# Optimization experiments

Measured on AMD Instinct MI355X. Metric: run time of the kernel, lower is better.

The kernel has to match this reference:

```python
import jax, jax.numpy as jnp
import numpy as np

B = 8192        # number of drug-cell pairs (graphs)
NPG = 32        # nodes per graph
EPG = 64        # directed edges per graph
N = B * NPG     # total nodes
E = B * EPG     # total edges
CELL = 908      # cell_inp_dim
BN_EPS = 1e-5


def _bn(x):
    # BatchNorm1d in training mode with gamma=1, beta=0 (fresh init), biased var
    m = x.mean(0)
    v = x.var(0)
    return (x - m) * jax.lax.rsqrt(v + BN_EPS)


def _lin_params(k, fan_in, fan_out):
    kw, _ = jax.random.split(k)
    w = jax.random.normal(kw, (fan_in, fan_out), jnp.float32) / np.sqrt(fan_in)
    b = jnp.zeros((fan_out,), jnp.float32)
    return w, b


_DIMS = [("ce_1", CELL, 516), ("ce_2", 516, 256), ("ce_3", 256, 128),
         ("g1_1", 9, 128), ("g1_2", 128, 128),
         ("g2_1", 128, 128), ("g2_2", 128, 128),
         ("d_1", 128, 128), ("d_2", 128, 128),
         ("f_1", 256, 128), ("f_2", 128, 64), ("f_3", 64, 1)]


def setup_inputs() -> dict:
    key = jax.random.key(0)
    ks = jax.random.split(key, 4 + len(_DIMS))
    inp = {}
    inp["cell"] = jax.random.normal(ks[0], (B, CELL), jnp.float32)
    inp["drug_x"] = jax.random.normal(ks[1], (N, 9), jnp.float32)
    g = jnp.arange(E) // EPG  # graph id per edge
    src = g * NPG + jax.random.randint(ks[2], (E,), 0, NPG)
    dst = g * NPG + jax.random.randint(ks[3], (E,), 0, NPG)
    inp["drug_edge_index"] = jnp.stack([src, dst]).astype(jnp.int32)
    inp["drug_batch"] = (jnp.arange(N) // NPG).astype(jnp.int32)
    for i, (nm, a, b) in enumerate(_DIMS):
        w, bb = _lin_params(ks[4 + i], a, b)
        inp[nm + "_w"] = w
        inp[nm + "_b"] = bb
    return inp


def _forward(cell, drug_x, src, dst, batch,
             ce_1_w, ce_1_b, ce_2_w, ce_2_b, ce_3_w, ce_3_b,
             g1_1_w, g1_1_b, g1_2_w, g1_2_b,
             g2_1_w, g2_1_b, g2_2_w, g2_2_b,
             d_1_w, d_1_b, d_2_w, d_2_b,
             f_1_w, f_1_b, f_2_w, f_2_b, f_3_w, f_3_b):
    # cell_emb branch (dropout = identity in eval/reference)
    c = jax.nn.relu(_bn(cell @ ce_1_w + ce_1_b))
    c = jax.nn.relu(_bn(c @ ce_2_w + ce_2_b))
    c = jax.nn.relu(_bn(c @ ce_3_w + ce_3_b))

    # GINConv 1: h = MLP((1+eps)*x + sum_{j in N(i)} x_j), eps=0
    agg = jax.ops.segment_sum(drug_x[src], dst, num_segments=N)
    h = drug_x + agg
    h = jax.nn.relu(_bn(h @ g1_1_w + g1_1_b)) @ g1_2_w + g1_2_b  # inner MLP: Lin-BN-ReLU-Lin
    h = _bn(jax.nn.relu(h))  # outer ReLU then BN (per Sequential order)

    # GINConv 2
    agg = jax.ops.segment_sum(h[src], dst, num_segments=N)
    h = h + agg
    h = jax.nn.relu(_bn(h @ g2_1_w + g2_1_b)) @ g2_2_w + g2_2_b
    h = _bn(jax.nn.relu(h))

    # global max pool over nodes of each graph -> [B, 128]
    p = jax.ops.segment_max(h, batch, num_segments=B)

    d = jax.nn.relu(_bn(p @ d_1_w + d_1_b))
    d = jax.nn.relu(d @ d_2_w + d_2_b)

    z = jnp.concatenate([c, d], axis=-1)  # [B, 256]
    z = jax.nn.elu(_bn(z @ f_1_w + f_1_b))
    z = jax.nn.elu(_bn(z @ f_2_w + f_2_b))
    y = (z @ f_3_w + f_3_b).reshape(B)
    return y


def reference(cell, drug_x, drug_edge_index, drug_batch,
              ce_1_w, ce_1_b, ce_2_w, ce_2_b, ce_3_w, ce_3_b,
              g1_1_w, g1_1_b, g1_2_w, g1_2_b,
              g2_1_w, g2_1_b, g2_2_w, g2_2_b,
              d_1_w, d_1_b, d_2_w, d_2_b,
              f_1_w, f_1_b, f_2_w, f_2_b, f_3_w, f_3_b):
    src, dst = drug_edge_index[0], drug_edge_index[1]
    return _forward(cell, drug_x, src, dst, drug_batch,
                    ce_1_w, ce_1_b, ce_2_w, ce_2_b, ce_3_w, ce_3_b,
                    g1_1_w, g1_1_b, g1_2_w, g1_2_b,
                    g2_1_w, g2_1_b, g2_2_w, g2_2_b,
                    d_1_w, d_1_b, d_2_w, d_2_b,
                    f_1_w, f_1_b, f_2_w, f_2_b, f_3_w, f_3_b)
```

## Files before the change

### kernel.cpp

```cpp
#include <hip/hip_runtime.h>
#include <hip/hip_bf16.h>
#include <math.h>

#define BGRAPH 8192
#define NPG 32
#define EPG 64
#define NNODE (BGRAPH * NPG)
#define NEDGE (BGRAPH * EPG)
#define CELLD 908
#define BN_EPS 1e-5f
#define ABF_STR 1024
#define C1_STR 640

typedef __attribute__((ext_vector_type(8))) short bf16x8;
typedef __attribute__((ext_vector_type(4))) float f32x4;
typedef __attribute__((ext_vector_type(4))) unsigned short us4;
typedef __attribute__((ext_vector_type(8))) unsigned short us8;

__device__ __forceinline__ unsigned short f2bf(float f)
{
    unsigned int u = __float_as_uint(f);
    u = (u + 0x7FFFu + ((u >> 16) & 1u)) >> 16;
    return (unsigned short)u;
}

__device__ __forceinline__ bf16x8 quant8(const float v[8])
{
    union { bf16x8 b; unsigned short u[8]; } fr;
    #pragma unroll
    for (int j = 0; j < 8; ++j) fr.u[j] = f2bf(v[j]);
    return fr.b;
}

__device__ __forceinline__ void bf2f8(bf16x8 b, float v[8])
{
    union { bf16x8 bb; unsigned short u[8]; } x; x.bb = b;
    #pragma unroll
    for (int j = 0; j < 8; ++j) v[j] = __uint_as_float((unsigned)x.u[j] << 16);
}

__device__ __forceinline__ float apply_in(float v, int mode, float mn, float iv)
{
    if (mode == 1)      { v = (v - mn) * iv; v = fmaxf(v, 0.f); }
    else if (mode == 2) { v = (v - mn) * iv; v = (v > 0.f) ? v : expm1f(v); }
    else if (mode == 3) { v = fmaxf(v, 0.f); v = (v - mn) * iv; }
    return v;
}

struct TransArgs {
    const float* w[11];
    unsigned short* wt[11];
    int K[11], N[11], ntN[11];
    int off[12];
};

__global__ void transpose_w(TransArgs a)
{
    __shared__ float t[64][65];
    int b = blockIdx.x, tid = threadIdx.x;
    int s = 0;
    while (s < 10 && b >= a.off[s + 1]) ++s;
    int t0 = b - a.off[s];
    int K = a.K[s], N = a.N[s], ntn = a.ntN[s];
    int kt = t0 / ntn, nt = t0 - kt * ntn;
    int k0 = kt * 64, n0 = nt * 64;
    const float* w = a.w[s];
    unsigned short* wt = a.wt[s];
    int c = tid & 63, rg = tid >> 6;
    #pragma unroll
    for (int i = 0; i < 16; ++i) {
        int rr = rg * 16 + i;
        int k = k0 + rr, n = n0 + c;
        t[c][rr] = (k < K && n < N) ? w[(size_t)k * N + n] : 0.f;
    }
    __syncthreads();
    #pragma unroll
    for (int i = 0; i < 16; ++i) {
        int rr = rg * 16 + i;
        int n = n0 + rr, k = k0 + c;
        if (n < N && k < K) wt[(size_t)n * K + k] = f2bf(t[rr][c]);
    }
}

struct SetupArgs {
    float* zb; int zTotal; int zBlocks;
    const int* src; const int* dst; int* row_start; int* col_idx;
};

__global__ void setup_all(SetupArgs a)
{
    int b = blockIdx.x;
    int tid = threadIdx.x;
    if (b < a.zBlocks) {
        int i = b * 256 + tid;
        if (i < a.zTotal) a.zb[i] = 0.f;
        return;
    }
    b -= a.zBlocks;
    __shared__ int cnt[4][32], fill[4][32], rsl[4][33];
    int gl = tid >> 6, e = tid & 63;
    int g = b * 4 + gl;
    if (e < 32) { cnt[gl][e] = 0; fill[gl][e] = 0; }
    __syncthreads();
    int s = a.src[g * EPG + e] - g * NPG;
    int d = a.dst[g * EPG + e] - g * NPG;
    atomicAdd(&cnt[gl][d], 1);
    __syncthreads();
    if (e == 0) {
        int acc = 0;
        for (int i = 0; i < 32; ++i) { rsl[gl][i] = acc; acc += cnt[gl][i]; }
        rsl[gl][32] = acc;
    }
    __syncthreads();
    int pos = rsl[gl][d] + atomicAdd(&fill[gl][d], 1);
    a.col_idx[g * EPG + pos] = s;
    if (e < 33) a.row_start[g * 33 + e] = rsl[gl][e];
}

__global__ void quant_cell(const float* __restrict__ cell, unsigned short* __restrict__ abf)
{
    int i = blockIdx.x * 256 + threadIdx.x;
    int row = i / (ABF_STR / 4), c4 = i - row * (ABF_STR / 4);
    int k = c4 * 4;
    us4 w = (us4){0, 0, 0, 0};
    if (k < CELLD) {
        float4 f = *(const float4*)&cell[(size_t)row * CELLD + k];
        w = (us4){ f2bf(f.x), f2bf(f.y), f2bf(f.z), f2bf(f.w) };
    }
    *(us4*)&abf[(size_t)row * ABF_STR + k] = w;
}

__global__ void quant_c1(const float* __restrict__ c1, const float* __restrict__ stats,
                         float inv_sM, unsigned short* __restrict__ out)
{
    int i = blockIdx.x * 256 + threadIdx.x;
    int row = i / (C1_STR / 4), c4 = i - row * (C1_STR / 4);
    int k = c4 * 4;
    us4 w = (us4){0, 0, 0, 0};
    if (k < 516) {
        float4 f = *(const float4*)&c1[(size_t)row * 516 + k];
        float v[4] = {f.x, f.y, f.z, f.w};
        #pragma unroll
        for (int j = 0; j < 4; ++j) {
            float s = stats[k + j], ss = stats[516 + k + j];
            float mn = s * inv_sM;
            float iv = rsqrtf(ss * inv_sM - mn * mn + BN_EPS);
            v[j] = fmaxf((v[j] - mn) * iv, 0.f);
        }
        w = (us4){ f2bf(v[0]), f2bf(v[1]), f2bf(v[2]), f2bf(v[3]) };
    }
    *(us4*)&out[(size_t)row * C1_STR + k] = w;
}

__global__ void reduce_stats(const float* __restrict__ part, int nrows, int nt,
                             float* __restrict__ out)
{
    int c = threadIdx.x;
    int per = nrows >> 6;
    int r0 = blockIdx.x * per;
    bool isq = (c >= 128);
    int cc = isq ? c - 128 : c;
    if (cc >= nt) return;
    float s = 0.f;
    for (int r = 0; r < per; ++r) s += part[(size_t)(r0 + r) * 256 + c];
    unsafeAtomicAdd(&out[(isq ? nt : 0) + cc], s);
}

#define HBS 136

__launch_bounds__(256)
__global__ void gin_s1(const float* __restrict__ drug_x,
                       const int* __restrict__ row_start,
                       const int* __restrict__ col_idx,
                       const unsigned short* __restrict__ W11,
                       const float* __restrict__ b11,
                       unsigned short* uout,
                       float* __restrict__ part)
{
    __shared__ __align__(16) unsigned short h[4 * 32 * HBS];
    __shared__ __align__(16) unsigned char ubuf[4096];
    __shared__ int rs[4][36];
    __shared__ int ci[4][64];

    unsigned short* w11l = (unsigned short*)ubuf;
    float* red = (float*)ubuf;

    int tid  = threadIdx.x;
    int wave = tid >> 6;
    int lane = tid & 63;
    int quad = lane >> 4;
    int l16  = lane & 15;
    int g0   = blockIdx.x * 4;
    unsigned short* hw = h + wave * (32 * HBS);
    float* xw = (float*)hw;

    for (int i = tid; i < 128 * 16; i += 256) {
        int n = i >> 4, k = i & 15;
        w11l[i] = (k < 9) ? W11[n * 9 + k] : (unsigned short)0;
    }
    if (tid < 132) {
        int gl = tid / 33, idx = tid - gl * 33;
        rs[gl][idx] = row_start[(g0 + gl) * 33 + idx];
    }
    {
        int gl = tid >> 6, e = tid & 63;
        ci[gl][e] = col_idx[(g0 + gl) * EPG + e];
    }
    {
        const float* xg = drug_x + (size_t)(g0 + wave) * 32 * 9;
        for (int i = lane; i < 32 * 16; i += 64) {
            int rr = i >> 4, c = i & 15;
            xw[i] = (c < 9) ? xg[rr * 9 + c] : 0.f;
        }
    }
    __syncthreads();

    f32x4 acc[2][8];
    #pragma unroll
    for (int i = 0; i < 2; ++i)
        #pragma unroll
        for (int j = 0; j < 8; ++j)
            acc[i][j] = (f32x4){0.f, 0.f, 0.f, 0.f};

    {
        bf16x8 af[2];
        #pragma unroll
        for (int mt = 0; mt < 2; ++mt) {
            int rowl = mt * 16 + l16;
            float v[8] = {0, 0, 0, 0, 0, 0, 0, 0};
            if (quad < 2) {
                float4 lo = *(const float4*)&xw[rowl * 16 + quad * 8];
                float4 hi = *(const float4*)&xw[rowl * 16 + quad * 8 + 4];
                v[0] = lo.x; v[1] = lo.y; v[2] = lo.z; v[3] = lo.w;
                v[4] = hi.x; v[5] = hi.y; v[6] = hi.z; v[7] = hi.w;
                int e0 = rs[wave][rowl], e1 = rs[wave][rowl + 1];
                for (int e = e0; e < e1; ++e) {
                    int sr = ci[wave][e];
                    float4 l2 = *(const float4*)&xw[sr * 16 + quad * 8];
                    float4 h2 = *(const float4*)&xw[sr * 16 + quad * 8 + 4];
                    v[0] += l2.x; v[1] += l2.y; v[2] += l2.z; v[3] += l2.w;
                    v[4] += h2.x; v[5] += h2.y; v[6] += h2.z; v[7] += h2.w;
                }
            }
            af[mt] = quant8(v);
        }
        #pragma unroll
        for (int nt = 0; nt < 8; ++nt) {
            bf16x8 b;
            if (quad < 2) b = *(const bf16x8*)(const void*)&w11l[(nt * 16 + l16) * 16 + quad * 8];
            else { float z[8] = {0,0,0,0,0,0,0,0}; b = quant8(z); }
            acc[0][nt] = __builtin_amdgcn_mfma_f32_16x16x32_bf16(af[0], b, acc[0][nt], 0, 0, 0);
            acc[1][nt] = __builtin_amdgcn_mfma_f32_16x16x32_bf16(af[1], b, acc[1][nt], 0, 0, 0);
        }
    }

    float ls[8], lq[8];
    unsigned short* ub = uout + (size_t)(g0 + wave) * 32 * 128;
    #pragma unroll
    for (int nt = 0; nt < 8; ++nt) {
        int col = nt * 16 + l16;
        float bv = b11[col];
        float s0 = 0.f, q0 = 0.f;
        #pragma unroll
        for (int mt = 0; mt < 2; ++mt) {
            int rb = mt * 16 + quad * 4;
            #pragma unroll
            for (int r = 0; r < 4; ++r) {
                float u = acc[mt][nt][r] + bv;
                ub[(size_t)(rb + r) * 128 + col] = f2bf(u);
                s0 += u; q0 += u * u;
            }
        }
        ls[nt] = s0; lq[nt] = q0;
    }
    __syncthreads();
    #pragma unroll
    for (int nt = 0; nt < 8; ++nt) {
        float s = ls[nt], q = lq[nt];
        s += __shfl_xor(s, 16); q += __shfl_xor(q, 16);
        s += __shfl_xor(s, 32); q += __shfl_xor(q, 32);
        if (quad == 0) {
            int col = nt * 16 + l16;
            red[(wave * 2 + 0) * 128 + col] = s;
            red[(wave * 2 + 1) * 128 + col] = q;
        }
    }
    __syncthreads();
    if (tid < 128) {
        float s = red[0 * 128 + tid] + red[2 * 128 + tid] + red[4 * 128 + tid] + red[6 * 128 + tid];
        float q = red[1 * 128 + tid] + red[3 * 128 + tid] + red[5 * 128 + tid] + red[7 * 128 + tid];
        part[(size_t)blockIdx.x * 256 + tid] = s;
        part[(size_t)blockIdx.x * 256 + 128 + tid] = q;
    }
}

__launch_bounds__(256)
__global__ void gin_s3f(const unsigned short* __restrict__ uin,
                        const int* __restrict__ row_start,
                        const int* __restrict__ col_idx,
                        const unsigned short* __restrict__ Wt,
                        const float* __restrict__ bias,
                        const float* __restrict__ in_stats, float inv_sM,
                        unsigned short* __restrict__ uout,
                        float* __restrict__ part)
{
    __shared__ __align__(16) unsigned short wsl[128 * 136];
    __shared__ float pmv[256];
    __shared__ int rs[2][33];
    __shared__ int ci[2][64];
    float* zt = (float*)wsl;

    int tid  = threadIdx.x;
    int wave = tid >> 6;
    int lane = tid & 63;
    int quad = lane >> 4;
    int l16  = lane & 15;
    int g0   = blockIdx.x * 2;
    int row0 = blockIdx.x * 64;

    if (tid < 128) {
        float s = in_stats[tid], ss = in_stats[128 + tid];
        float mn = s * inv_sM;
        pmv[tid] = mn;
        pmv[128 + tid] = rsqrtf(ss * inv_sM - mn * mn + BN_EPS);
    }
    if (tid < 66) {
        int gl = tid / 33, idx = tid - gl * 33;
        rs[gl][idx] = row_start[(g0 + gl) * 33 + idx];
    }
    if (tid >= 128) {
        int t = tid - 128;
        ci[t >> 6][t & 63] = col_idx[(g0 + (t >> 6)) * EPG + (t & 63)];
    }
    for (int i = tid; i < 128 * 32; i += 256) {
        int n = i >> 5, k = (i & 31) * 4;
        *(us4*)&wsl[n * 136 + k] = *(const us4*)&Wt[(size_t)n * 128 + k];
    }
    __syncthreads();

    bf16x8 afrag[4];
    {
        const unsigned short* ap = uin + (size_t)(row0 + wave * 16 + l16) * 128;
        #pragma unroll
        for (int ks = 0; ks < 4; ++ks) {
            int kb = ks * 32 + quad * 8;
            float v[8];
            bf2f8(*(const bf16x8*)(const void*)&ap[kb], v);
            #pragma unroll
            for (int j = 0; j < 8; ++j)
                v[j] = (fmaxf(v[j], 0.f) - pmv[kb + j]) * pmv[128 + kb + j];
            afrag[ks] = quant8(v);
        }
    }

    f32x4 acc[8];
    #pragma unroll
    for (int j = 0; j < 8; ++j) acc[j] = (f32x4){0.f, 0.f, 0.f, 0.f};
    #pragma unroll
    for (int ks = 0; ks < 4; ++ks) {
        int kb = ks * 32 + quad * 8;
        #pragma unroll
        for (int nt = 0; nt < 8; ++nt) {
            bf16x8 b = *(const bf16x8*)(const void*)&wsl[(nt * 16 + l16) * 136 + kb];
            acc[nt] = __builtin_amdgcn_mfma_f32_16x16x32_bf16(afrag[ks], b, acc[nt], 0, 0, 0);
        }
    }
    __syncthreads();

    #pragma unroll
    for (int nt = 0; nt < 8; ++nt) {
        int col = nt * 16 + l16;
        #pragma unroll
        for (int r = 0; r < 4; ++r)
            zt[(wave * 16 + quad * 4 + r) * 132 + col] = acc[nt][r];
    }
    __syncthreads();

    float sv[4] = {0.f, 0.f, 0.f, 0.f}, qv[4] = {0.f, 0.f, 0.f, 0.f};
    {
        int c4  = (tid & 31) * 4;
        int rg  = tid >> 5;
        int hh  = rg >> 2;
        int rb0 = (rg & 3) * 8;
        float4 bv = *(const float4*)&bias[c4];
        unsigned short* ub = uout + (size_t)row0 * 128;
        for (int rr = 0; rr < 8; ++rr) {
            int r = rb0 + rr;
            int lr = hh * 32 + r;
            float4 val = *(const float4*)&zt[lr * 132 + c4];
            int e0 = rs[hh][r], e1 = rs[hh][r + 1];
            for (int e = e0; e < e1; ++e) {
                float4 zz = *(const float4*)&zt[(hh * 32 + ci[hh][e]) * 132 + c4];
                val.x += zz.x; val.y += zz.y; val.z += zz.z; val.w += zz.w;
            }
            float u0 = val.x + bv.x, u1 = val.y + bv.y;
            float u2 = val.z + bv.z, u3 = val.w + bv.w;
            *(us4*)&ub[(size_t)lr * 128 + c4] =
                (us4){ f2bf(u0), f2bf(u1), f2bf(u2), f2bf(u3) };
            sv[0] += u0; sv[1] += u1; sv[2] += u2; sv[3] += u3;
            qv[0] += u0 * u0; qv[1] += u1 * u1; qv[2] += u2 * u2; qv[3] += u3 * u3;
        }
    }
    __syncthreads();
    {
        int c4 = (tid & 31) * 4, rg = tid >> 5;
        #pragma unroll
        for (int j = 0; j < 4; ++j) {
            zt[rg * 128 + c4 + j] = sv[j];
            zt[1024 + rg * 128 + c4 + j] = qv[j];
        }
    }
    __syncthreads();
    if (tid < 128) {
        float s = 0.f, q = 0.f;
        #pragma unroll
        for (int rg = 0; rg < 8; ++rg) {
            s += zt[rg * 128 + tid];
            q += zt[1024 + rg * 128 + tid];
        }
        part[(size_t)blockIdx.x * 256 + tid] = s;
        part[(size_t)blockIdx.x * 256 + 128 + tid] = q;
    }
}

template<int DO_POOL>
__launch_bounds__(256)
__global__ void gin_lin(const unsigned short* __restrict__ uin,
                        const unsigned short* __restrict__ Wt,
                        const float* __restrict__ bias,
                        const float* __restrict__ in_stats, float inv_sM,
                        unsigned short* uout,
                        float* __restrict__ part,
                        float* __restrict__ pool_out)
{
    __shared__ __align__(16) unsigned short Ws_l[128 * 136];
    __shared__ float pmv[256];
    __shared__ float red[4][2][128];

    int tid  = threadIdx.x;
    int wave = tid >> 6;
    int lane = tid & 63;
    int quad = lane >> 4;
    int l16  = lane & 15;
    int row0 = blockIdx.x * 64;

    for (int i = tid; i < 128 * 32; i += 256) {
        int n = i >> 5, k = (i & 31) * 4;
        *(us4*)&Ws_l[n * 136 + k] = *(const us4*)&Wt[(size_t)n * 128 + k];
    }
    if (tid < 128) {
        float s = in_stats[tid], ss = in_stats[128 + tid];
        float mn = s * inv_sM;
        pmv[tid] = mn;
        pmv[128 + tid] = rsqrtf(ss * inv_sM - mn * mn + BN_EPS);
    }
    __syncthreads();

    bf16x8 afrag[4];
    {
        const unsigned short* ap = uin + (size_t)(row0 + wave * 16 + l16) * 128;
        #pragma unroll
        for (int ks = 0; ks < 4; ++ks) {
            int kb = ks * 32 + quad * 8;
            float v[8];
            bf2f8(*(const bf16x8*)(const void*)&ap[kb], v);
            #pragma unroll
            for (int j = 0; j < 8; ++j)
                v[j] = fmaxf((v[j] - pmv[kb + j]) * pmv[128 + kb + j], 0.f);
            afrag[ks] = quant8(v);
        }
    }

    f32x4 acc[8];
    #pragma unroll
    for (int j = 0; j < 8; ++j) acc[j] = (f32x4){0.f, 0.f, 0.f, 0.f};
    #pragma unroll
    for (int ks = 0; ks < 4; ++ks) {
        int kb = ks * 32 + quad * 8;
        #pragma unroll
        for (int nt = 0; nt < 8; ++nt) {
            bf16x8 b = *(const bf16x8*)(const void*)&Ws_l[(nt * 16 + l16) * 136 + kb];
            acc[nt] = __builtin_amdgcn_mfma_f32_16x16x32_bf16(afrag[ks], b, acc[nt], 0, 0, 0);
        }
    }

    float ls[8], lq[8], lm[8];
    #pragma unroll
    for (int nt = 0; nt < 8; ++nt) {
        int col = nt * 16 + l16;
        float bv = bias[col];
        int rb = row0 + wave * 16 + quad * 4;
        float s0 = 0.f, q0 = 0.f, mx = -INFINITY;
        #pragma unroll
        for (int r = 0; r < 4; ++r) {
            float u = acc[nt][r] + bv;
            float ru = fmaxf(u, 0.f);
            s0 += ru; q0 += ru * ru;
            if (DO_POOL) mx = fmaxf(mx, ru);
            else uout[(size_t)(rb + r) * 128 + col] = f2bf(u);
        }
        ls[nt] = s0; lq[nt] = q0; lm[nt] = mx;
    }

    #pragma unroll
    for (int nt = 0; nt < 8; ++nt) {
        float s = ls[nt], q = lq[nt];
        s += __shfl_xor(s, 16); q += __shfl_xor(q, 16);
        s += __shfl_xor(s, 32); q += __shfl_xor(q, 32);
        if (quad == 0) {
            red[wave][0][nt * 16 + l16] = s;
            red[wave][1][nt * 16 + l16] = q;
        }
    }
    __syncthreads();
    if (tid < 128) {
        float s = red[0][0][tid] + red[1][0][tid] + red[2][0][tid] + red[3][0][tid];
        float q = red[0][1][tid] + red[1][1][tid] + red[2][1][tid] + red[3][1][tid];
        part[(size_t)blockIdx.x * 256 + tid] = s;
        part[(size_t)blockIdx.x * 256 + 128 + tid] = q;
    }
    if (DO_POOL) {
        __syncthreads();
        #pragma unroll
        for (int nt = 0; nt < 8; ++nt) {
            float m = lm[nt];
            m = fmaxf(m, __shfl_xor(m, 16));
            m = fmaxf(m, __shfl_xor(m, 32));
            if (quad == 0) red[wave][0][nt * 16 + l16] = m;
        }
        __syncthreads();
        {
            int gi = tid >> 7, col = tid & 127;
            float m = fmaxf(red[gi * 2][0][col], red[gi * 2 + 1][0][col]);
            pool_out[(size_t)((row0 >> 5) + gi) * 128 + col] = m;
        }
    }
}

template<int KSTEPS, int NT>
__launch_bounds__(256)
__global__ void gemm_rB(const float* __restrict__ A, const float* __restrict__ A2,
                        int lda, int K, int stats_K, int ksplit,
                        const unsigned short* __restrict__ Wt,
                        const float* __restrict__ bias, float* __restrict__ C,
                        const float* __restrict__ in_stats, float inv_sM, int in_mode,
                        float* __restrict__ part, int stats_mode, int out_act)
{
    constexpr int NSUBW = NT / 64;
    __shared__ float pm[KSTEPS * 32], pv[KSTEPS * 32];

    int tid  = threadIdx.x;
    int wave = tid >> 6;
    int lane = tid & 63;
    int quad = lane >> 4;
    int l16  = lane & 15;
    int m0   = blockIdx.x * 16;

    if (in_mode) {
        for (int k = tid; k < KSTEPS * 32; k += 256) {
            float mn = 0.f, iv = 1.f;
            if (k < stats_K) {
                float s = in_stats[k], ss = in_stats[stats_K + k];
                mn = s * inv_sM;
                float vr = ss * inv_sM - mn * mn;
                iv = rsqrtf(vr + BN_EPS);
            }
            pm[k] = mn; pv[k] = iv;
        }
        __syncthreads();
    }

    bf16x8 afrag[KSTEPS];
    {
        int row = m0 + l16;
        const float* ap = A + (size_t)row * lda;
        #pragma unroll
        for (int ks = 0; ks < KSTEPS; ++ks) {
            int kb = ks * 32 + quad * 8;
            float v[8];
            #pragma unroll
            for (int hh = 0; hh < 2; ++hh) {
                int k = kb + hh * 4;
                const float* p = (k >= ksplit) ? &A2[(size_t)row * 128 + (k - 128)]
                                               : &ap[k];
                float4 f = *(const float4*)p;
                v[hh * 4 + 0] = f.x; v[hh * 4 + 1] = f.y;
                v[hh * 4 + 2] = f.z; v[hh * 4 + 3] = f.w;
            }
            if (in_mode) {
                #pragma unroll
                for (int j = 0; j < 8; ++j)
                    v[j] = apply_in(v[j], in_mode, pm[kb + j], pv[kb + j]);
            }
            afrag[ks] = quant8(v);
        }
    }

    f32x4 acc[NSUBW];
    #pragma unroll
    for (int j = 0; j < NSUBW; ++j) acc[j] = (f32x4){0.f, 0.f, 0.f, 0.f};

    #pragma unroll
    for (int ks = 0; ks < KSTEPS; ++ks) {
        #pragma unroll
        for (int nt = 0; nt < NSUBW; ++nt) {
            int wrow = (wave * NSUBW + nt) * 16 + l16;
            bf16x8 b = *(const bf16x8*)(const void*)&Wt[(size_t)wrow * K + ks * 32 + quad * 8];
            acc[nt] = __builtin_amdgcn_mfma_f32_16x16x32_bf16(afrag[ks], b, acc[nt], 0, 0, 0);
        }
    }

    float ls[NSUBW], lq[NSUBW];
    #pragma unroll
    for (int nt = 0; nt < NSUBW; ++nt) { ls[nt] = 0.f; lq[nt] = 0.f; }

    #pragma unroll
    for (int nt = 0; nt < NSUBW; ++nt) {
        int col = (wave * NSUBW + nt) * 16 + l16;
        float bv = bias[col];
        int rbase = m0 + quad * 4;
        #pragma unroll
        for (int r = 0; r < 4; ++r) {
            float u = acc[nt][r] + bv;
            if (C) {
                float wv = out_act ? fmaxf(u, 0.f) : u;
                C[(size_t)(rbase + r) * NT + col] = wv;
            }
            if (stats_mode) {
                float s = (stats_mode == 2) ? fmaxf(u, 0.f) : u;
                ls[nt] += s; lq[nt] += s * s;
            }
        }
    }

    if (stats_mode) {
        #pragma unroll
        for (int nt = 0; nt < NSUBW; ++nt) {
            float s = ls[nt], q = lq[nt];
            s += __shfl_xor(s, 16); q += __shfl_xor(q, 16);
            s += __shfl_xor(s, 32); q += __shfl_xor(q, 32);
            if (quad == 0) {
                int col = (wave * NSUBW + nt) * 16 + l16;
                part[(size_t)blockIdx.x * 256 + col] = s;
                part[(size_t)blockIdx.x * 256 + 128 + col] = q;
            }
        }
    }
}

template<int NT>
__launch_bounds__(256)
__global__ void gemm_cell(const unsigned short* __restrict__ Abf, int abf_str,
                          const unsigned short* __restrict__ Wt,
                          const float* __restrict__ bias, float* __restrict__ C,
                          int K, int N, float* __restrict__ out_stats)
{
    constexpr int NSUB = NT / 32;
    constexpr int WITEMS = NT * 32 / 256;
    __shared__ __align__(16) unsigned short As_l[32 * 136];
    __shared__ __align__(16) unsigned short Ws_l[NT * 136];
    __shared__ float red[2][2][NT];

    int tid = threadIdx.x;
    int wave = tid >> 6;
    int lane = tid & 63;
    int quad = lane >> 4;
    int l16 = lane & 15;
    int mhalf = wave & 1, nhalf = wave >> 1;
    int m0 = blockIdx.x * 32, n0 = blockIdx.y * NT;

    us8 aReg[2];
    us4 wReg[WITEMS];

    auto loadA = [&](int k0) {
        #pragma unroll
        for (int t = 0; t < 2; ++t) {
            int i = t * 256 + tid;
            int row = i >> 4, c8 = (i & 15) * 8;
            aReg[t] = *(const us8*)&Abf[(size_t)(m0 + row) * abf_str + k0 + c8];
        }
    };
    auto loadW = [&](int k0) {
        #pragma unroll
        for (int t = 0; t < WITEMS; ++t) {
            int i = t * 256 + tid;
            int nn = i >> 5, kt = i & 31;
            int k = k0 + kt * 4;
            int gn = n0 + nn;
            us4 w4 = (us4){0, 0, 0, 0};
            if (gn < N && k < K) w4 = *(const us4*)&Wt[(size_t)gn * K + k];
            wReg[t] = w4;
        }
    };
    auto storeAW = [&]() {
        #pragma unroll
        for (int t = 0; t < 2; ++t) {
            int i = t * 256 + tid;
            int row = i >> 4, c8 = (i & 15) * 8;
            *(us8*)&As_l[row * 136 + c8] = aReg[t];
        }
        #pragma unroll
        for (int t = 0; t < WITEMS; ++t) {
            int i = t * 256 + tid;
            int nn = i >> 5, kt = i & 31;
            *(us4*)&Ws_l[nn * 136 + kt * 4] = wReg[t];
        }
    };

    f32x4 acc[NSUB];
    #pragma unroll
    for (int j = 0; j < NSUB; ++j) acc[j] = (f32x4){0.f, 0.f, 0.f, 0.f};

    int nch = (K + 127) >> 7;
    loadA(0); loadW(0);
    for (int c = 0; c < nch; ++c) {
        storeAW();
        if (c + 1 < nch) { loadA((c + 1) * 128); loadW((c + 1) * 128); }
        __syncthreads();
        #pragma unroll
        for (int ks = 0; ks < 4; ++ks) {
            bf16x8 a = *(const bf16x8*)(const void*)
                &As_l[(mhalf * 16 + l16) * 136 + ks * 32 + quad * 8];
            #pragma unroll
            for (int nt = 0; nt < NSUB; ++nt) {
                bf16x8 b = *(const bf16x8*)(const void*)
                    &Ws_l[(nhalf * (NT / 2) + nt * 16 + l16) * 136 + ks * 32 + quad * 8];
                acc[nt] = __builtin_amdgcn_mfma_f32_16x16x32_bf16(a, b, acc[nt], 0, 0, 0);
            }
        }
        __syncthreads();
    }

    float ls[NSUB], lq[NSUB];
    #pragma unroll
    for (int nt = 0; nt < NSUB; ++nt) { ls[nt] = 0.f; lq[nt] = 0.f; }

    #pragma unroll
    for (int nt = 0; nt < NSUB; ++nt) {
        int col = n0 + nhalf * (NT / 2) + nt * 16 + l16;
        if (col < N) {
            float bv = bias[col];
            int rbase = m0 + mhalf * 16 + quad * 4;
            #pragma unroll
            for (int r = 0; r < 4; ++r) {
                float u = acc[nt][r] + bv;
                C[(size_t)(rbase + r) * N + col] = u;
                ls[nt] += u; lq[nt] += u * u;
            }
        }
    }

    #pragma unroll
    for (int nt = 0; nt < NSUB; ++nt) {
        float s = ls[nt], q = lq[nt];
        s += __shfl_xor(s, 16); q += __shfl_xor(q, 16);
        s += __shfl_xor(s, 32); q += __shfl_xor(q, 32);
        if (quad == 0) {
            int lc = nhalf * (NT / 2) + nt * 16 + l16;
            red[mhalf][0][lc] = s;
            red[mhalf][1][lc] = q;
        }
    }
    __syncthreads();
    if (tid < NT) {
        int col = n0 + tid;
        if (col < N) {
            float s = red[0][0][tid] + red[1][0][tid];
            float q = red[0][1][tid] + red[1][1][tid];
            unsafeAtomicAdd(&out_stats[col], s);
            unsafeAtomicAdd(&out_stats[N + col], q);
        }
    }
}

__global__ void final_dot(const float* __restrict__ u, const float* __restrict__ w,
                          const float* __restrict__ b, float* __restrict__ y,
                          const float* __restrict__ stats, float inv_sM)
{
    __shared__ float pmv[64], piv[64], sw[64];
    int tid = threadIdx.x;
    if (tid < 64) {
        float s = stats[tid], ss = stats[64 + tid];
        float mn = s * inv_sM;
        float vr = ss * inv_sM - mn * mn;
        pmv[tid] = mn;
        piv[tid] = rsqrtf(vr + BN_EPS);
        sw[tid] = w[tid];
    }
    __syncthreads();
    int i = blockIdx.x * blockDim.x + tid;
    if (i >= BGRAPH) return;
    float acc = 0.f;
    #pragma unroll
    for (int k = 0; k < 64; ++k) {
        float v = (u[(size_t)i * 64 + k] - pmv[k]) * piv[k];
        v = (v > 0.f) ? v : expm1f(v);
        acc += v * sw[k];
    }
    y[i] = acc + b[0];
}

extern "C" void kernel_launch(void* const* d_in, const int* in_sizes, int n_in,
                              void* d_out, int out_size, void* d_ws, size_t ws_size,
                              hipStream_t stream)
{
    const float* cell   = (const float*)d_in[0];
    const float* drug_x = (const float*)d_in[1];
    const int*   eidx   = (const int*)d_in[2];
    const float* ce1w = (const float*)d_in[4];  const float* ce1b = (const float*)d_in[5];
    const float* ce2w = (const float*)d_in[6];  const float* ce2b = (const float*)d_in[7];
    const float* ce3w = (const float*)d_in[8];  const float* ce3b = (const float*)d_in[9];
    const float* g11w = (const float*)d_in[10]; const float* g11b = (const float*)d_in[11];
    const float* g12w = (const float*)d_in[12]; const float* g12b = (const float*)d_in[13];
    const float* g21w = (const float*)d_in[14]; const float* g21b = (const float*)d_in[15];
    const float* g22w = (const float*)d_in[16]; const float* g22b = (const float*)d_in[17];
    const float* d1w  = (const float*)d_in[18]; const float* d1b  = (const float*)d_in[19];
    const float* d2w  = (const float*)d_in[20]; const float* d2b  = (const float*)d_in[21];
    const float* f1w  = (const float*)d_in[22]; const float* f1b  = (const float*)d_in[23];
    const float* f2w  = (const float*)d_in[24]; const float* f2b  = (const float*)d_in[25];
    const float* f3w  = (const float*)d_in[26]; const float* f3b  = (const float*)d_in[27];

    const int* src = eidx;
    const int* dst = eidx + NEDGE;
    float* out = (float*)d_out;

    const float INV_N = 1.f / (float)NNODE;
    const float INV_B = 1.f / (float)BGRAPH;
    const int KBIG = 1 << 30;

    float* ws = (float*)d_ws;
    unsigned short* ubg = (unsigned short*)ws;
    float* pbuf = ws + (size_t)NNODE * 64;
    float* sb   = pbuf + (size_t)BGRAPH * 128;
    unsigned short* wtb = (unsigned short*)(sb + 10 * 1032);
    auto ST = [&](int i) { return sb + (size_t)i * 1032; };
    float* st_u1    = ST(0);
    float* st_u2rel = ST(1);
    float* st_u3    = ST(2);
    float* st_u4rel = ST(3);
    float* st_c1    = ST(4);
    float* st_c2    = ST(5);
    float* st_c3    = ST(6);
    float* st_d1    = ST(7);
    float* st_f1    = ST(8);
    float* st_f2    = ST(9);

    float* c1    = ws;
    float* c2    = c1 + (size_t)BGRAPH * 516;
    float* c3u   = c2 + (size_t)BGRAPH * 256;
    float* dbuf  = c3u + (size_t)BGRAPH * 128;
    float* d2buf = dbuf + (size_t)BGRAPH * 128;
    float* f1o   = d2buf + (size_t)BGRAPH * 128;
    float* f2o   = f1o + (size_t)BGRAPH * 128;

    struct WDef { const float* w; int K; int N; };
    WDef wd[11] = {
        {ce1w, CELLD, 516}, {ce2w, 516, 256}, {ce3w, 256, 128},
        {g11w, 9, 128}, {g12w, 128, 128}, {g21w, 128, 128}, {g22w, 128, 128},
        {d1w, 128, 128}, {d2w, 128, 128}, {f1w, 256, 128}, {f2w, 128, 64}
    };
    TransArgs ta;
    int off = 0;
    unsigned short* wt[11];
    ta.off[0] = 0;
    for (int i = 0; i < 11; ++i) {
        wt[i] = wtb + off;
        ta.w[i] = wd[i].w; ta.wt[i] = wt[i];
        ta.K[i] = wd[i].K; ta.N[i] = wd[i].N;
        ta.ntN[i] = (wd[i].N + 63) / 64;
        ta.off[i + 1] = ta.off[i] + ((wd[i].K + 63) / 64) * ta.ntN[i];
        off += wd[i].K * wd[i].N;
    }

    SetupArgs sa;
    sa.zb = sb; sa.zTotal = 10 * 1032; sa.zBlocks = (10 * 1032 + 255) / 256;
    sa.src = src; sa.dst = dst;

    int csr_off = (off + 7) & ~7;
    int* row_start = (int*)(wtb + csr_off);
    int* col_idx   = row_start + (size_t)BGRAPH * 33;
    float* part = (float*)(col_idx + (size_t)NEDGE);
    unsigned short* Abf  = (unsigned short*)(part + (size_t)4096 * 256);
    unsigned short* C1bf = Abf + (size_t)BGRAPH * ABF_STR;
    sa.row_start = row_start; sa.col_idx = col_idx;

    transpose_w<<<ta.off[11], 256, 0, stream>>>(ta);
    setup_all<<<sa.zBlocks + BGRAPH / 4, 256, 0, stream>>>(sa);

    gin_s1<<<BGRAPH / 4, 256, 0, stream>>>(
        drug_x, row_start, col_idx, wt[3], g11b, ubg, part);
    reduce_stats<<<64, 256, 0, stream>>>(part, BGRAPH / 4, 128, st_u1);

    gin_lin<0><<<NNODE / 64, 256, 0, stream>>>(
        ubg, wt[4], g12b, st_u1, INV_N, ubg, part, nullptr);
    reduce_stats<<<64, 256, 0, stream>>>(part, NNODE / 64, 128, st_u2rel);

    gin_s3f<<<BGRAPH / 2, 256, 0, stream>>>(
        ubg, row_start, col_idx, wt[5], g21b, st_u2rel, INV_N, ubg, part);
    reduce_stats<<<64, 256, 0, stream>>>(part, BGRAPH / 2, 128, st_u3);

    gin_lin<1><<<NNODE / 64, 256, 0, stream>>>(
        ubg, wt[6], g22b, st_u3, INV_N, nullptr, part, pbuf);
    reduce_stats<<<64, 256, 0, stream>>>(part, NNODE / 64, 128, st_u4rel);

    quant_cell<<<(BGRAPH * (ABF_STR / 4)) / 256, 256, 0, stream>>>(cell, Abf);
    gemm_cell<128><<<dim3(BGRAPH / 32, 5), 256, 0, stream>>>(
        Abf, ABF_STR, wt[0], ce1b, c1, CELLD, 516, st_c1);
    quant_c1<<<(BGRAPH * (C1_STR / 4)) / 256, 256, 0, stream>>>(c1, st_c1, INV_B, C1bf);
    gemm_cell<64><<<dim3(BGRAPH / 32, 4), 256, 0, stream>>>(
        C1bf, C1_STR, wt[1], ce2b, c2, 516, 256, st_c2);
    gemm_rB<8, 128><<<BGRAPH / 16, 256, 0, stream>>>(
        c2, nullptr, 256, 256, 256, KBIG, wt[2], ce3b, c3u,
        st_c2, INV_B, 1, part, 1, 0);
    reduce_stats<<<64, 256, 0, stream>>>(part, BGRAPH / 16, 128, st_c3);

    gemm_rB<4, 128><<<BGRAPH / 16, 256, 0, stream>>>(
        pbuf, nullptr, 128, 128, 128, KBIG, wt[7], d1b, dbuf,
        st_u4rel, INV_N, 3, part, 1, 0);
    reduce_stats<<<64, 256, 0, stream>>>(part, BGRAPH / 16, 128, st_d1);
    gemm_rB<4, 128><<<BGRAPH / 16, 256, 0, stream>>>(
        dbuf, nullptr, 128, 128, 128, KBIG, wt[8], d2b, d2buf,
        st_d1, INV_B, 1, part, 0, 1);

    gemm_rB<8, 128><<<BGRAPH / 16, 256, 0, stream>>>(
        c3u, d2buf, 128, 256, 128, 128, wt[9], f1b, f1o,
        st_c3, INV_B, 1, part, 1, 0);
    reduce_stats<<<64, 256, 0, stream>>>(part, BGRAPH / 16, 128, st_f1);
    gemm_rB<4, 64><<<BGRAPH / 16, 256, 0, stream>>>(
        f1o, nullptr, 128, 128, 128, KBIG, wt[10], f2b, f2o,
        st_f1, INV_B, 2, part, 1, 0);
    reduce_stats<<<64, 256, 0, stream>>>(part, BGRAPH / 16, 64, st_f2);
    final_dot<<<BGRAPH / 256, 256, 0, stream>>>(f2o, f3w, f3b, out, st_f2, INV_B);
}
```

Measured before the change: 525.9 us.

## Co-schedule independent drug GIN and cell MLP stages in merged kernel launches

Kernels are turned into device functions over a shared-memory struct, then pairs of independent stages from the drug-graph branch and the cell-embedding branch are launched as one grid and split by block index. Weight transpose, CSR setup and cell quantization are also merged into one prep kernel. The aim is fewer launches and better GPU fill by overlapping the independent branches, with a second partial-stats buffer so the two branches do not collide. In exchange, the merged kernels share a smem size set by the larger member, which can lower occupancy for the smaller one, and the buffer aliasing needs care.

```diff
diff --git a/kernel.cpp b/kernel.cpp
--- a/kernel.cpp
+++ b/kernel.cpp
@@ -11,6 +11,7 @@
 #define BN_EPS 1e-5f
 #define ABF_STR 1024
 #define C1_STR 640
+#define HBS 136
 
 typedef __attribute__((ext_vector_type(8))) short bf16x8;
 typedef __attribute__((ext_vector_type(4))) float f32x4;
@@ -53,11 +54,11 @@
     int K[11], N[11], ntN[11];
     int off[12];
 };
-
-__global__ void transpose_w(TransArgs a)
-{
-    __shared__ float t[64][65];
-    int b = blockIdx.x, tid = threadIdx.x;
+struct TransSmem { float t[64][65]; };
+
+__device__ void dev_transpose(TransSmem* sm, int b, const TransArgs& a)
+{
+    int tid = threadIdx.x;
     int s = 0;
     while (s < 10 && b >= a.off[s + 1]) ++s;
     int t0 = b - a.off[s];
@@ -71,14 +72,14 @@
     for (int i = 0; i < 16; ++i) {
         int rr = rg * 16 + i;
         int k = k0 + rr, n = n0 + c;
-        t[c][rr] = (k < K && n < N) ? w[(size_t)k * N + n] : 0.f;
+        sm->t[c][rr] = (k < K && n < N) ? w[(size_t)k * N + n] : 0.f;
     }
     __syncthreads();
     #pragma unroll
     for (int i = 0; i < 16; ++i) {
         int rr = rg * 16 + i;
         int n = n0 + rr, k = k0 + c;
-        if (n < N && k < K) wt[(size_t)n * K + k] = f2bf(t[rr][c]);
+        if (n < N && k < K) wt[(size_t)n * K + k] = f2bf(sm->t[rr][c]);
     }
 }
 
@@ -86,10 +87,10 @@
     float* zb; int zTotal; int zBlocks;
     const int* src; const int* dst; int* row_start; int* col_idx;
 };
-
-__global__ void setup_all(SetupArgs a)
-{
-    int b = blockIdx.x;
+struct SetupSmem { int cnt[4][32]; int fill[4][32]; int rsl[4][33]; };
+
+__device__ void dev_setup(SetupSmem* sm, int b, const SetupArgs& a)
+{
     int tid = threadIdx.x;
     if (b < a.zBlocks) {
         int i = b * 256 + tid;
@@ -97,29 +98,29 @@
         return;
     }
     b -= a.zBlocks;
-    __shared__ int cnt[4][32], fill[4][32], rsl[4][33];
     int gl = tid >> 6, e = tid & 63;
     int g = b * 4 + gl;
-    if (e < 32) { cnt[gl][e] = 0; fill[gl][e] = 0; }
+    if (e < 32) { sm->cnt[gl][e] = 0; sm->fill[gl][e] = 0; }
     __syncthreads();
     int s = a.src[g * EPG + e] - g * NPG;
     int d = a.dst[g * EPG + e] - g * NPG;
-    atomicAdd(&cnt[gl][d], 1);
+    atomicAdd(&sm->cnt[gl][d], 1);
     __syncthreads();
     if (e == 0) {
         int acc = 0;
-        for (int i = 0; i < 32; ++i) { rsl[gl][i] = acc; acc += cnt[gl][i]; }
-        rsl[gl][32] = acc;
-    }
-    __syncthreads();
-    int pos = rsl[gl][d] + atomicAdd(&fill[gl][d], 1);
+        for (int i = 0; i < 32; ++i) { sm->rsl[gl][i] = acc; acc += sm->cnt[gl][i]; }
+        sm->rsl[gl][32] = acc;
+    }
+    __syncthreads();
+    int pos = sm->rsl[gl][d] + atomicAdd(&sm->fill[gl][d], 1);
     a.col_idx[g * EPG + pos] = s;
-    if (e < 33) a.row_start[g * 33 + e] = rsl[gl][e];
-}
-
-__global__ void quant_cell(const float* __restrict__ cell, unsigned short* __restrict__ abf)
-{
-    int i = blockIdx.x * 256 + threadIdx.x;
+    if (e < 33) a.row_start[g * 33 + e] = sm->rsl[gl][e];
+}
+
+__device__ void dev_quant_cell(int bid, const float* __restrict__ cell,
+                               unsigned short* __restrict__ abf)
+{
+    int i = bid * 256 + threadIdx.x;
     int row = i / (ABF_STR / 4), c4 = i - row * (ABF_STR / 4);
     int k = c4 * 4;
     us4 w = (us4){0, 0, 0, 0};
@@ -130,10 +131,11 @@
     *(us4*)&abf[(size_t)row * ABF_STR + k] = w;
 }
 
-__global__ void quant_c1(const float* __restrict__ c1, const float* __restrict__ stats,
-                         float inv_sM, unsigned short* __restrict__ out)
-{
-    int i = blockIdx.x * 256 + threadIdx.x;
+__device__ void dev_quant_c1(int bid, const float* __restrict__ c1,
+                             const float* __restrict__ stats, float inv_sM,
+                             unsigned short* __restrict__ out)
+{
+    int i = bid * 256 + threadIdx.x;
     int row = i / (C1_STR / 4), c4 = i - row * (C1_STR / 4);
     int k = c4 * 4;
     us4 w = (us4){0, 0, 0, 0};
@@ -152,12 +154,12 @@
     *(us4*)&out[(size_t)row * C1_STR + k] = w;
 }
 
-__global__ void reduce_stats(const float* __restrict__ part, int nrows, int nt,
-                             float* __restrict__ out)
+__device__ void dev_reduce(int bid, const float* __restrict__ part, int nrows,
+                           int nt, float* __restrict__ out)
 {
     int c = threadIdx.x;
     int per = nrows >> 6;
-    int r0 = blockIdx.x * per;
+    int r0 = bid * per;
     bool isq = (c >= 128);
     int cc = isq ? c - 128 : c;
     if (cc >= nt) return;
@@ -166,32 +168,31 @@
     unsafeAtomicAdd(&out[(isq ? nt : 0) + cc], s);
 }
 
-#define HBS 136
-
-__launch_bounds__(256)
-__global__ void gin_s1(const float* __restrict__ drug_x,
-                       const int* __restrict__ row_start,
-                       const int* __restrict__ col_idx,
-                       const unsigned short* __restrict__ W11,
-                       const float* __restrict__ b11,
-                       unsigned short* uout,
-                       float* __restrict__ part)
-{
-    __shared__ __align__(16) unsigned short h[4 * 32 * HBS];
-    __shared__ __align__(16) unsigned char ubuf[4096];
-    __shared__ int rs[4][36];
-    __shared__ int ci[4][64];
-
-    unsigned short* w11l = (unsigned short*)ubuf;
-    float* red = (float*)ubuf;
+struct S1Smem {
+    unsigned short h[4 * 32 * HBS];
+    unsigned char ubuf[4096];
+    int rs[4][36];
+    int ci[4][64];
+};
+
+__device__ void dev_gin_s1(S1Smem* sm, int bid,
+                           const float* __restrict__ drug_x,
+                           const int* __restrict__ row_start,
+                           const int* __restrict__ col_idx,
+                           const unsigned short* __restrict__ W11,
+                           const float* __restrict__ b11,
+                           unsigned short* uout, float* __restrict__ part)
+{
+    unsigned short* w11l = (unsigned short*)sm->ubuf;
+    float* red = (float*)sm->ubuf;
 
     int tid  = threadIdx.x;
     int wave = tid >> 6;
     int lane = tid & 63;
     int quad = lane >> 4;
     int l16  = lane & 15;
-    int g0   = blockIdx.x * 4;
-    unsigned short* hw = h + wave * (32 * HBS);
+    int g0   = bid * 4;
+    unsigned short* hw = sm->h + wave * (32 * HBS);
     float* xw = (float*)hw;
 
     for (int i = tid; i < 128 * 16; i += 256) {
@@ -200,11 +201,11 @@
     }
     if (tid < 132) {
         int gl = tid / 33, idx = tid - gl * 33;
-        rs[gl][idx] = row_start[(g0 + gl) * 33 + idx];
+        sm->rs[gl][idx] = row_start[(g0 + gl) * 33 + idx];
     }
     {
         int gl = tid >> 6, e = tid & 63;
-        ci[gl][e] = col_idx[(g0 + gl) * EPG + e];
+        sm->ci[gl][e] = col_idx[(g0 + gl) * EPG + e];
     }
     {
         const float* xg = drug_x + (size_t)(g0 + wave) * 32 * 9;
@@ -233,9 +234,9 @@
                 float4 hi = *(const float4*)&xw[rowl * 16 + quad * 8 + 4];
                 v[0] = lo.x; v[1] = lo.y; v[2] = lo.z; v[3] = lo.w;
                 v[4] = hi.x; v[5] = hi.y; v[6] = hi.z; v[7] = hi.w;
-                int e0 = rs[wave][rowl], e1 = rs[wave][rowl + 1];
+                int e0 = sm->rs[wave][rowl], e1 = sm->rs[wave][rowl + 1];
                 for (int e = e0; e < e1; ++e) {
-                    int sr = ci[wave][e];
+                    int sr = sm->ci[wave][e];
                     float4 l2 = *(const float4*)&xw[sr * 16 + quad * 8];
                     float4 h2 = *(const float4*)&xw[sr * 16 + quad * 8 + 4];
                     v[0] += l2.x; v[1] += l2.y; v[2] += l2.z; v[3] += l2.w;
@@ -289,52 +290,55 @@
     if (tid < 128) {
         float s = red[0 * 128 + tid] + red[2 * 128 + tid] + red[4 * 128 + tid] + red[6 * 128 + tid];
         float q = red[1 * 128 + tid] + red[3 * 128 + tid] + red[5 * 128 + tid] + red[7 * 128 + tid];
-        part[(size_t)blockIdx.x * 256 + tid] = s;
-        part[(size_t)blockIdx.x * 256 + 128 + tid] = q;
-    }
-}
-
-__launch_bounds__(256)
-__global__ void gin_s3f(const unsigned short* __restrict__ uin,
-                        const int* __restrict__ row_start,
-                        const int* __restrict__ col_idx,
-                        const unsigned short* __restrict__ Wt,
-                        const float* __restrict__ bias,
-                        const float* __restrict__ in_stats, float inv_sM,
-                        unsigned short* __restrict__ uout,
-                        float* __restrict__ part)
-{
-    __shared__ __align__(16) unsigned short wsl[128 * 136];
-    __shared__ float pmv[256];
-    __shared__ int rs[2][33];
-    __shared__ int ci[2][64];
-    float* zt = (float*)wsl;
+        part[(size_t)bid * 256 + tid] = s;
+        part[(size_t)bid * 256 + 128 + tid] = q;
+    }
+}
+
+struct S3fSmem {
+    unsigned short wsl[128 * 136];
+    float pmv[256];
+    int rs[2][33];
+    int ci[2][64];
+};
+
+__device__ void dev_gin_s3f(S3fSmem* sm, int bid,
+                            const unsigned short* __restrict__ uin,
+                            const int* __restrict__ row_start,
+                            const int* __restrict__ col_idx,
+                            const unsigned short* __restrict__ Wt,
+                            const float* __restrict__ bias,
+                            const float* __restrict__ in_stats, float inv_sM,
+                            unsigned short* __restrict__ uout,
+                            float* __restrict__ part)
+{
+    float* zt = (float*)sm->wsl;
 
     int tid  = threadIdx.x;
     int wave = tid >> 6;
     int lane = tid & 63;
     int quad = lane >> 4;
     int l16  = lane & 15;
-    int g0   = blockIdx.x * 2;
-    int row0 = blockIdx.x * 64;
+    int g0   = bid * 2;
+    int row0 = bid * 64;
 
     if (tid < 128) {
         float s = in_stats[tid], ss = in_stats[128 + tid];
         float mn = s * inv_sM;
-        pmv[tid] = mn;
-        pmv[128 + tid] = rsqrtf(ss * inv_sM - mn * mn + BN_EPS);
+        sm->pmv[tid] = mn;
+        sm->pmv[128 + tid] = rsqrtf(ss * inv_sM - mn * mn + BN_EPS);
     }
     if (tid < 66) {
         int gl = tid / 33, idx = tid - gl * 33;
-        rs[gl][idx] = row_start[(g0 + gl) * 33 + idx];
+        sm->rs[gl][idx] = row_start[(g0 + gl) * 33 + idx];
     }
     if (tid >= 128) {
         int t = tid - 128;
-        ci[t >> 6][t & 63] = col_idx[(g0 + (t >> 6)) * EPG + (t & 63)];
+        sm->ci[t >> 6][t & 63] = col_idx[(g0 + (t >> 6)) * EPG + (t & 63)];
     }
     for (int i = tid; i < 128 * 32; i += 256) {
         int n = i >> 5, k = (i & 31) * 4;
-        *(us4*)&wsl[n * 136 + k] = *(const us4*)&Wt[(size_t)n * 128 + k];
+        *(us4*)&sm->wsl[n * 136 + k] = *(const us4*)&Wt[(size_t)n * 128 + k];
     }
     __syncthreads();
 
@@ -348,7 +352,7 @@
             bf2f8(*(const bf16x8*)(const void*)&ap[kb], v);
             #pragma unroll
             for (int j = 0; j < 8; ++j)
-                v[j] = (fmaxf(v[j], 0.f) - pmv[kb + j]) * pmv[128 + kb + j];
+                v[j] = (fmaxf(v[j], 0.f) - sm->pmv[kb + j]) * sm->pmv[128 + kb + j];
             afrag[ks] = quant8(v);
         }
     }
@@ -361,7 +365,7 @@
         int kb = ks * 32 + quad * 8;
         #pragma unroll
         for (int nt = 0; nt < 8; ++nt) {
-            bf16x8 b = *(const bf16x8*)(const void*)&wsl[(nt * 16 + l16) * 136 + kb];
+            bf16x8 b = *(const bf16x8*)(const void*)&sm->wsl[(nt * 16 + l16) * 136 + kb];
             acc[nt] = __builtin_amdgcn_mfma_f32_16x16x32_bf16(afrag[ks], b, acc[nt], 0, 0, 0);
         }
     }
@@ -388,9 +392,9 @@
             int r = rb0 + rr;
             int lr = hh * 32 + r;
             float4 val = *(const float4*)&zt[lr * 132 + c4];
-            int e0 = rs[hh][r], e1 = rs[hh][r + 1];
+            int e0 = sm->rs[hh][r], e1 = sm->rs[hh][r + 1];
             for (int e = e0; e < e1; ++e) {
-                float4 zz = *(const float4*)&zt[(hh * 32 + ci[hh][e]) * 132 + c4];
+                float4 zz = *(const float4*)&zt[(hh * 32 + sm->ci[hh][e]) * 132 + c4];
                 val.x += zz.x; val.y += zz.y; val.z += zz.z; val.w += zz.w;
             }
             float u0 = val.x + bv.x, u1 = val.y + bv.y;
@@ -418,41 +422,43 @@
             s += zt[rg * 128 + tid];
             q += zt[1024 + rg * 128 + tid];
         }
-        part[(size_t)blockIdx.x * 256 + tid] = s;
-        part[(size_t)blockIdx.x * 256 + 128 + tid] = q;
-    }
-}
+        part[(size_t)bid * 256 + tid] = s;
+        part[(size_t)bid * 256 + 128 + tid] = q;
+    }
+}
+
+struct LinSmem {
+    unsigned short Ws_l[128 * 136];
+    float pmv[256];
+    float red[4][2][128];
+};
 
 template<int DO_POOL>
-__launch_bounds__(256)
-__global__ void gin_lin(const unsigned short* __restrict__ uin,
-                        const unsigned short* __restrict__ Wt,
-                        const float* __restrict__ bias,
-                        const float* __restrict__ in_stats, float inv_sM,
-                        unsigned short* uout,
-                        float* __restrict__ part,
-                        float* __restrict__ pool_out)
-{
-    __shared__ __align__(16) unsigned short Ws_l[128 * 136];
-    __shared__ float pmv[256];
-    __shared__ float red[4][2][128];
-
+__device__ void dev_gin_lin(LinSmem* sm, int bid,
+                            const unsigned short* __restrict__ uin,
+                            const unsigned short* __restrict__ Wt,
+                            const float* __restrict__ bias,
+                            const float* __restrict__ in_stats, float inv_sM,
+                            unsigned short* uout,
+                            float* __restrict__ part,
+                            float* __restrict__ pool_out)
+{
     int tid  = threadIdx.x;
     int wave = tid >> 6;
     int lane = tid & 63;
     int quad = lane >> 4;
     int l16  = lane & 15;
-    int row0 = blockIdx.x * 64;
+    int row0 = bid * 64;
 
     for (int i = tid; i < 128 * 32; i += 256) {
         int n = i >> 5, k = (i & 31) * 4;
-        *(us4*)&Ws_l[n * 136 + k] = *(const us4*)&Wt[(size_t)n * 128 + k];
+        *(us4*)&sm->Ws_l[n * 136 + k] = *(const us4*)&Wt[(size_t)n * 128 + k];
     }
     if (tid < 128) {
         float s = in_stats[tid], ss = in_stats[128 + tid];
         float mn = s * inv_sM;
-        pmv[tid] = mn;
-        pmv[128 + tid] = rsqrtf(ss * inv_sM - mn * mn + BN_EPS);
+        sm->pmv[tid] = mn;
+        sm->pmv[128 + tid] = rsqrtf(ss * inv_sM - mn * mn + BN_EPS);
     }
     __syncthreads();
 
@@ -466,7 +472,7 @@
             bf2f8(*(const bf16x8*)(const void*)&ap[kb], v);
             #pragma unroll
             for (int j = 0; j < 8; ++j)
-                v[j] = fmaxf((v[j] - pmv[kb + j]) * pmv[128 + kb + j], 0.f);
+                v[j] = fmaxf((v[j] - sm->pmv[kb + j]) * sm->pmv[128 + kb + j], 0.f);
             afrag[ks] = quant8(v);
         }
     }
@@ -479,7 +485,7 @@
         int kb = ks * 32 + quad * 8;
         #pragma unroll
         for (int nt = 0; nt < 8; ++nt) {
-            bf16x8 b = *(const bf16x8*)(const void*)&Ws_l[(nt * 16 + l16) * 136 + kb];
+            bf16x8 b = *(const bf16x8*)(const void*)&sm->Ws_l[(nt * 16 + l16) * 136 + kb];
             acc[nt] = __builtin_amdgcn_mfma_f32_16x16x32_bf16(afrag[ks], b, acc[nt], 0, 0, 0);
         }
     }
@@ -508,16 +514,16 @@
         s += __shfl_xor(s, 16); q += __shfl_xor(q, 16);
         s += __shfl_xor(s, 32); q += __shfl_xor(q, 32);
         if (quad == 0) {
-            red[wave][0][nt * 16 + l16] = s;
-            red[wave][1][nt * 16 + l16] = q;
+            sm->red[wave][0][nt * 16 + l16] = s;
+            sm->red[wave][1][nt * 16 + l16] = q;
         }
     }
     __syncthreads();
     if (tid < 128) {
-        float s = red[0][0][tid] + red[1][0][tid] + red[2][0][tid] + red[3][0][tid];
-        float q = red[0][1][tid] + red[1][1][tid] + red[2][1][tid] + red[3][1][tid];
-        part[(size_t)blockIdx.x * 256 + tid] = s;
-        part[(size_t)blockIdx.x * 256 + 128 + tid] = q;
+        float s = sm->red[0][0][tid] + sm->red[1][0][tid] + sm->red[2][0][tid] + sm->red[3][0][tid];
+        float q = sm->red[0][1][tid] + sm->red[1][1][tid] + sm->red[2][1][tid] + sm->red[3][1][tid];
+        part[(size_t)bid * 256 + tid] = s;
+        part[(size_t)bid * 256 + 128 + tid] = q;
     }
     if (DO_POOL) {
         __syncthreads();
@@ -526,35 +532,35 @@
             float m = lm[nt];
             m = fmaxf(m, __shfl_xor(m, 16));
             m = fmaxf(m, __shfl_xor(m, 32));
-            if (quad == 0) red[wave][0][nt * 16 + l16] = m;
+            if (quad == 0) sm->red[wave][0][nt * 16 + l16] = m;
         }
         __syncthreads();
         {
             int gi = tid >> 7, col = tid & 127;
-            float m = fmaxf(red[gi * 2][0][col], red[gi * 2 + 1][0][col]);
+            float m = fmaxf(sm->red[gi * 2][0][col], sm->red[gi * 2 + 1][0][col]);
             pool_out[(size_t)((row0 >> 5) + gi) * 128 + col] = m;
         }
     }
 }
 
+struct RBSmem { float pm[256]; float pv[256]; };
+
 template<int KSTEPS, int NT>
-__launch_bounds__(256)
-__global__ void gemm_rB(const float* __restrict__ A, const float* __restrict__ A2,
-                        int lda, int K, int stats_K, int ksplit,
-                        const unsigned short* __restrict__ Wt,
-                        const float* __restrict__ bias, float* __restrict__ C,
-                        const float* __restrict__ in_stats, float inv_sM, int in_mode,
-                        float* __restrict__ part, int stats_mode, int out_act)
+__device__ void dev_rB(RBSmem* sm, int bid,
+                       const float* __restrict__ A, const float* __restrict__ A2,
+                       int lda, int K, int stats_K, int ksplit,
+                       const unsigned short* __restrict__ Wt,
+                       const float* __restrict__ bias, float* __restrict__ C,
+                       const float* __restrict__ in_stats, float inv_sM, int in_mode,
+                       float* __restrict__ part, int stats_mode, int out_act)
 {
     constexpr int NSUBW = NT / 64;
-    __shared__ float pm[KSTEPS * 32], pv[KSTEPS * 32];
-
     int tid  = threadIdx.x;
     int wave = tid >> 6;
     int lane = tid & 63;
     int quad = lane >> 4;
     int l16  = lane & 15;
-    int m0   = blockIdx.x * 16;
+    int m0   = bid * 16;
 
     if (in_mode) {
         for (int k = tid; k < KSTEPS * 32; k += 256) {
@@ -565,7 +571,7 @@
                 float vr = ss * inv_sM - mn * mn;
                 iv = rsqrtf(vr + BN_EPS);
             }
-            pm[k] = mn; pv[k] = iv;
+            sm->pm[k] = mn; sm->pv[k] = iv;
         }
         __syncthreads();
     }
@@ -590,7 +596,7 @@
             if (in_mode) {
                 #pragma unroll
                 for (int j = 0; j < 8; ++j)
-                    v[j] = apply_in(v[j], in_mode, pm[kb + j], pv[kb + j]);
+                    v[j] = apply_in(v[j], in_mode, sm->pm[kb + j], sm->pv[kb + j]);
             }
             afrag[ks] = quant8(v);
         }
@@ -641,33 +647,36 @@
             s += __shfl_xor(s, 32); q += __shfl_xor(q, 32);
             if (quad == 0) {
                 int col = (wave * NSUBW + nt) * 16 + l16;
-                part[(size_t)blockIdx.x * 256 + col] = s;
-                part[(size_t)blockIdx.x * 256 + 128 + col] = q;
+                part[(size_t)bid * 256 + col] = s;
+                part[(size_t)bid * 256 + 128 + col] = q;
             }
         }
     }
 }
 
 template<int NT>
-__launch_bounds__(256)
-__global__ void gemm_cell(const unsigned short* __restrict__ Abf, int abf_str,
-                          const unsigned short* __restrict__ Wt,
-                          const float* __restrict__ bias, float* __restrict__ C,
-                          int K, int N, float* __restrict__ out_stats)
+struct CellSmem {
+    unsigned short As_l[32 * 136];
+    unsigned short Ws_l[NT * 136];
+    float red[2][2][NT];
+};
+
+template<int NT>
+__device__ void dev_gemm_cell(CellSmem<NT>* sm, int bid,
+                              const unsigned short* __restrict__ Abf, int abf_str,
+                              const unsigned short* __restrict__ Wt,
+                              const float* __restrict__ bias, float* __restrict__ C,
+                              int K, int N, float* __restrict__ out_stats)
 {
     constexpr int NSUB = NT / 32;
     constexpr int WITEMS = NT * 32 / 256;
-    __shared__ __align__(16) unsigned short As_l[32 * 136];
-    __shared__ __align__(16) unsigned short Ws_l[NT * 136];
-    __shared__ float red[2][2][NT];
-
     int tid = threadIdx.x;
     int wave = tid >> 6;
     int lane = tid & 63;
     int quad = lane >> 4;
     int l16 = lane & 15;
     int mhalf = wave & 1, nhalf = wave >> 1;
-    int m0 = blockIdx.x * 32, n0 = blockIdx.y * NT;
+    int m0 = (bid & 255) * 32, n0 = (bid >> 8) * NT;
 
     us8 aReg[2];
     us4 wReg[WITEMS];
@@ -697,13 +706,13 @@
         for (int t = 0; t < 2; ++t) {
             int i = t * 256 + tid;
             int row = i >> 4, c8 = (i & 15) * 8;
-            *(us8*)&As_l[row * 136 + c8] = aReg[t];
+            *(us8*)&sm->As_l[row * 136 + c8] = aReg[t];
         }
         #pragma unroll
         for (int t = 0; t < WITEMS; ++t) {
             int i = t * 256 + tid;
             int nn = i >> 5, kt = i & 31;
-            *(us4*)&Ws_l[nn * 136 + kt * 4] = wReg[t];
+            *(us4*)&sm->Ws_l[nn * 136 + kt * 4] = wReg[t];
         }
     };
 
@@ -720,11 +729,11 @@
         #pragma unroll
         for (int ks = 0; ks < 4; ++ks) {
             bf16x8 a = *(const bf16x8*)(const void*)
-                &As_l[(mhalf * 16 + l16) * 136 + ks * 32 + quad * 8];
+                &sm->As_l[(mhalf * 16 + l16) * 136 + ks * 32 + quad * 8];
             #pragma unroll
             for (int nt = 0; nt < NSUB; ++nt) {
                 bf16x8 b = *(const bf16x8*)(const void*)
-                    &Ws_l[(nhalf * (NT / 2) + nt * 16 + l16) * 136 + ks * 32 + quad * 8];
+                    &sm->Ws_l[(nhalf * (NT / 2) + nt * 16 + l16) * 136 + ks * 32 + quad * 8];
                 acc[nt] = __builtin_amdgcn_mfma_f32_16x16x32_bf16(a, b, acc[nt], 0, 0, 0);
             }
         }
@@ -757,20 +766,136 @@
         s += __shfl_xor(s, 32); q += __shfl_xor(q, 32);
         if (quad == 0) {
             int lc = nhalf * (NT / 2) + nt * 16 + l16;
-            red[mhalf][0][lc] = s;
-            red[mhalf][1][lc] = q;
+            sm->red[mhalf][0][lc] = s;
+            sm->red[mhalf][1][lc] = q;
         }
     }
     __syncthreads();
     if (tid < NT) {
         int col = n0 + tid;
         if (col < N) {
-            float s = red[0][0][tid] + red[1][0][tid];
-            float q = red[0][1][tid] + red[1][1][tid];
+            float s = sm->red[0][0][tid] + sm->red[1][0][tid];
+            float q = sm->red[0][1][tid] + sm->red[1][1][tid];
             unsafeAtomicAdd(&out_stats[col], s);
             unsafeAtomicAdd(&out_stats[N + col], q);
         }
     }
+}
+
+__global__ __launch_bounds__(256)
+void prep(TransArgs ta, SetupArgs sa, const float* cell, unsigned short* abf,
+          int nbT, int nbZC)
+{
+    __shared__ __align__(16) char smem[sizeof(TransSmem)];
+    int b = blockIdx.x;
+    if (b < nbT) { dev_transpose((TransSmem*)smem, b, ta); return; }
+    b -= nbT;
+    if (b < nbZC) { dev_setup((SetupSmem*)smem, b, sa); return; }
+    b -= nbZC;
+    dev_quant_cell(b, cell, abf);
+}
+
+__global__ __launch_bounds__(256)
+void f_s1_ce1(const float* drug_x, const int* row_start, const int* col_idx,
+              const unsigned short* W11, const float* b11,
+              unsigned short* uout, float* partA,
+              const unsigned short* Abf, const unsigned short* Wt0,
+              const float* ce1b, float* c1, float* st_c1, int nb1)
+{
+    constexpr size_t SZ = sizeof(S1Smem) > sizeof(CellSmem<128>)
+                        ? sizeof(S1Smem) : sizeof(CellSmem<128>);
+    __shared__ __align__(16) char smem[SZ];
+    int b = blockIdx.x;
+    if (b < nb1)
+        dev_gin_s1((S1Smem*)smem, b, drug_x, row_start, col_idx, W11, b11, uout, partA);
+    else
+        dev_gemm_cell<128>((CellSmem<128>*)smem, b - nb1, Abf, ABF_STR, Wt0,
+                           ce1b, c1, CELLD, 516, st_c1);
+}
+
+__global__ __launch_bounds__(256)
+void f_red_qc1(const float* partA, int nrows, float* out,
+               const float* c1, const float* st_c1, float inv_B,
+               unsigned short* c1bf, int nb1)
+{
+    int b = blockIdx.x;
+    if (b < nb1) dev_reduce(b, partA, nrows, 128, out);
+    else dev_quant_c1(b - nb1, c1, st_c1, inv_B, c1bf);
+}
+
+__global__ __launch_bounds__(256)
+void f_lin0_ce2(const unsigned short* uin, const unsigned short* Wt4,
+                const float* g12b, const float* st_u1, float inv_N,
+                unsigned short* uout, float* partA,
+                const unsigned short* C1bf, const unsigned short* Wt1,
+                const float* ce2b, float* c2, float* st_c2, int nb1)
+{
+    constexpr size_t SZ = sizeof(LinSmem) > sizeof(CellSmem<64>)
+                        ? sizeof(LinSmem) : sizeof(CellSmem<64>);
+    __shared__ __align__(16) char smem[SZ];
+    int b = blockIdx.x;
+    if (b < nb1)
+        dev_gin_lin<0>((LinSmem*)smem, b, uin, Wt4, g12b, st_u1, inv_N,
+                       uout, partA, nullptr);
+    else
+        dev_gemm_cell<64>((CellSmem<64>*)smem, b - nb1, C1bf, C1_STR, Wt1,
+                          ce2b, c2, 516, 256, st_c2);
+}
+
+__global__ __launch_bounds__(256)
+void f_red_ce3(const float* partA, int nrows, float* out,
+               const float* c2, const unsigned short* Wt2, const float* ce3b,
+               float* c3u, const float* st_c2, float inv_B, float* partB, int nb1)
+{
+    __shared__ __align__(16) char smem[sizeof(RBSmem)];
+    int b = blockIdx.x;
+    if (b < nb1) dev_reduce(b, partA, nrows, 128, out);
+    else dev_rB<8, 128>((RBSmem*)smem, b - nb1, c2, nullptr, 256, 256, 256,
+                        1 << 30, Wt2, ce3b, c3u, st_c2, inv_B, 1, partB, 1, 0);
+}
+
+__global__ __launch_bounds__(256)
+void f_s3f_red(const unsigned short* uin, const int* row_start, const int* col_idx,
+               const unsigned short* Wt5, const float* g21b,
+               const float* st_u2rel, float inv_N, unsigned short* uout,
+               float* partA, const float* partB, int nrowsB, float* st_c3, int nb1)
+{
+    __shared__ __align__(16) char smem[sizeof(S3fSmem)];
+    int b = blockIdx.x;
+    if (b < nb1)
+        dev_gin_s3f((S3fSmem*)smem, b, uin, row_start, col_idx, Wt5, g21b,
+                    st_u2rel, inv_N, uout, partA);
+    else
+        dev_reduce(b - nb1, partB, nrowsB, 128, st_c3);
+}
+
+__global__ __launch_bounds__(256)
+void reduce_stats(const float* __restrict__ part, int nrows, int nt,
+                  float* __restrict__ out)
+{
+    dev_reduce(blockIdx.x, part, nrows, nt, out);
+}
+
+__global__ __launch_bounds__(256)
+void gin_lin1(const unsigned short* uin, const unsigned short* Wt,
+              const float* bias, const float* in_stats, float inv_sM,
+              float* part, float* pool_out)
+{
+    __shared__ __align__(16) char smem[sizeof(LinSmem)];
+    dev_gin_lin<1>((LinSmem*)smem, blockIdx.x, uin, Wt, bias, in_stats, inv_sM,
+                   nullptr, part, pool_out);
+}
+
+template<int KSTEPS, int NT>
+__global__ __launch_bounds__(256)
+void gemm_rB(const float* A, const float* A2, int lda, int K, int stats_K,
+             int ksplit, const unsigned short* Wt, const float* bias, float* C,
+             const float* in_stats, float inv_sM, int in_mode,
+             float* part, int stats_mode, int out_act)
+{
+    __shared__ __align__(16) char smem[sizeof(RBSmem)];
+    dev_rB<KSTEPS, NT>((RBSmem*)smem, blockIdx.x, A, A2, lda, K, stats_K, ksplit,
+                       Wt, bias, C, in_stats, inv_sM, in_mode, part, stats_mode, out_act);
 }
 
 __global__ void final_dot(const float* __restrict__ u, const float* __restrict__ w,
@@ -844,14 +969,6 @@
     float* st_d1    = ST(7);
     float* st_f1    = ST(8);
     float* st_f2    = ST(9);
-
-    float* c1    = ws;
-    float* c2    = c1 + (size_t)BGRAPH * 516;
-    float* c3u   = c2 + (size_t)BGRAPH * 256;
-    float* dbuf  = c3u + (size_t)BGRAPH * 128;
-    float* d2buf = dbuf + (size_t)BGRAPH * 128;
-    float* f1o   = d2buf + (size_t)BGRAPH * 128;
-    float* f2o   = f1o + (size_t)BGRAPH * 128;
 
     struct WDef { const float* w; int K; int N; };
     WDef wd[11] = {
@@ -879,56 +996,64 @@
     int csr_off = (off + 7) & ~7;
     int* row_start = (int*)(wtb + csr_off);
     int* col_idx   = row_start + (size_t)BGRAPH * 33;
-    float* part = (float*)(col_idx + (size_t)NEDGE);
-    unsigned short* Abf  = (unsigned short*)(part + (size_t)4096 * 256);
+    float* partA = (float*)(col_idx + (size_t)NEDGE);
+    float* partB = partA + (size_t)4096 * 256;
+    unsigned short* Abf  = (unsigned short*)(partB + (size_t)512 * 256);
     unsigned short* C1bf = Abf + (size_t)BGRAPH * ABF_STR;
+    float* cellws = (float*)(C1bf + (size_t)BGRAPH * C1_STR);
+    float* c1  = cellws;
+    float* c2  = cellws;
+    float* c3u = cellws + (size_t)BGRAPH * 256;
+    float* dbuf  = ws;
+    float* d2buf = dbuf + (size_t)BGRAPH * 128;
+    float* f1o   = d2buf + (size_t)BGRAPH * 128;
+    float* f2o   = f1o + (size_t)BGRAPH * 128;
     sa.row_start = row_start; sa.col_idx = col_idx;
 
-    transpose_w<<<ta.off[11], 256, 0, stream>>>(ta);
-    setup_all<<<sa.zBlocks + BGRAPH / 4, 256, 0, stream>>>(sa);
-
-    gin_s1<<<BGRAPH / 4, 256, 0, stream>>>(
-        drug_x, row_start, col_idx, wt[3], g11b, ubg, part);
-    reduce_stats<<<64, 256, 0, stream>>>(part, BGRAPH / 4, 128, st_u1);
-
-    gin_lin<0><<<NNODE / 64, 256, 0, stream>>>(
-        ubg, wt[4], g12b, st_u1, INV_N, ubg, part, nullptr);
-    reduce_stats<<<64, 256, 0, stream>>>(part, NNODE / 64, 128, st_u2rel);
-
-    gin_s3f<<<BGRAPH / 2, 256, 0, stream>>>(
-        ubg, row_start, col_idx, wt[5], g21b, st_u2rel, INV_N, ubg, part);
-    reduce_stats<<<64, 256, 0, stream>>>(part, BGRAPH / 2, 128, st_u3);
-
-    gin_lin<1><<<NNODE / 64, 256, 0, stream>>>(
-        ubg, wt[6], g22b, st_u3, INV_N, nullptr, part, pbuf);
-    reduce_stats<<<64, 256, 0, stream>>>(part, NNODE / 64, 128, st_u4rel);
-
-    quant_cell<<<(BGRAPH * (ABF_STR / 4)) / 256, 256, 0, stream>>>(cell, Abf);
-    gemm_cell<128><<<dim3(BGRAPH / 32, 5), 256, 0, stream>>>(
-        Abf, ABF_STR, wt[0], ce1b, c1, CELLD, 516, st_c1);
-    quant_c1<<<(BGRAPH * (C1_STR / 4)) / 256, 256, 0, stream>>>(c1, st_c1, INV_B, C1bf);
-    gemm_cell<64><<<dim3(BGRAPH / 32, 4), 256, 0, stream>>>(
-        C1bf, C1_STR, wt[1], ce2b, c2, 516, 256, st_c2);
-    gemm_rB<8, 128><<<BGRAPH / 16, 256, 0, stream>>>(
-        c2, nullptr, 256, 256, 256, KBIG, wt[2], ce3b, c3u,
-        st_c2, INV_B, 1, part, 1, 0);
-    reduce_stats<<<64, 256, 0, stream>>>(part, BGRAPH / 16, 128, st_c3);
+    int nbT = ta.off[11];
+    int nbZC = sa.zBlocks + BGRAPH / 4;
+
+    prep<<<nbT + nbZC + 8192, 256, 0, stream>>>(ta, sa, cell, Abf, nbT, nbZC);
+
+    f_s1_ce1<<<2048 + 1280, 256, 0, stream>>>(
+        drug_x, row_start, col_idx, wt[3], g11b, ubg, partA,
+        Abf, wt[0], ce1b, c1, st_c1, 2048);
+
+    f_red_qc1<<<64 + 5120, 256, 0, stream>>>(
+        partA, BGRAPH / 4, st_u1, c1, st_c1, INV_B, C1bf, 64);
+
+    f_lin0_ce2<<<4096 + 1024, 256, 0, stream>>>(
+        ubg, wt[4], g12b, st_u1, INV_N, ubg, partA,
+        C1bf, wt[1], ce2b, c2, st_c2, 4096);
+
+    f_red_ce3<<<64 + 512, 256, 0, stream>>>(
+        partA, NNODE / 64, st_u2rel, c2, wt[2], ce3b, c3u, st_c2, INV_B, partB, 64);
+
+    f_s3f_red<<<4096 + 64, 256, 0, stream>>>(
+        ubg, row_start, col_idx, wt[5], g21b, st_u2rel, INV_N, ubg, partA,
+        partB, BGRAPH / 16, st_c3, 4096);
+
+    reduce_stats<<<64, 256, 0, stream>>>(partA, BGRAPH / 2, 128, st_u3);
+
+    gin_lin1<<<NNODE / 64, 256, 0, stream>>>(
+        ubg, wt[6], g22b, st_u3, INV_N, partA, pbuf);
+    reduce_stats<<<64, 256, 0, stream>>>(partA, NNODE / 64, 128, st_u4rel);
 
     gemm_rB<4, 128><<<BGRAPH / 16, 256, 0, stream>>>(
         pbuf, nullptr, 128, 128, 128, KBIG, wt[7], d1b, dbuf,
-        st_u4rel, INV_N, 3, part, 1, 0);
-    reduce_stats<<<64, 256, 0, stream>>>(part, BGRAPH / 16, 128, st_d1);
+        st_u4rel, INV_N, 3, partA, 1, 0);
+    reduce_stats<<<64, 256, 0, stream>>>(partA, BGRAPH / 16, 128, st_d1);
     gemm_rB<4, 128><<<BGRAPH / 16, 256, 0, stream>>>(
         dbuf, nullptr, 128, 128, 128, KBIG, wt[8], d2b, d2buf,
-        st_d1, INV_B, 1, part, 0, 1);
+        st_d1, INV_B, 1, partA, 0, 1);
 
     gemm_rB<8, 128><<<BGRAPH / 16, 256, 0, stream>>>(
         c3u, d2buf, 128, 256, 128, 128, wt[9], f1b, f1o,
-        st_c3, INV_B, 1, part, 1, 0);
-    reduce_stats<<<64, 256, 0, stream>>>(part, BGRAPH / 16, 128, st_f1);
+        st_c3, INV_B, 1, partA, 1, 0);
+    reduce_stats<<<64, 256, 0, stream>>>(partA, BGRAPH / 16, 128, st_f1);
     gemm_rB<4, 64><<<BGRAPH / 16, 256, 0, stream>>>(
         f1o, nullptr, 128, 128, 128, KBIG, wt[10], f2b, f2o,
-        st_f1, INV_B, 2, part, 1, 0);
-    reduce_stats<<<64, 256, 0, stream>>>(part, BGRAPH / 16, 64, st_f2);
+        st_f1, INV_B, 2, partA, 1, 0);
+    reduce_stats<<<64, 256, 0, stream>>>(partA, BGRAPH / 16, 64, st_f2);
     final_dot<<<BGRAPH / 256, 256, 0, stream>>>(f2o, f3w, f3b, out, st_f2, INV_B);
 }
```

Result: no change. 517.1 us (median of 2 runs) (-1.7%).
